# Kernel tuning notes

Hardware: AMD Instinct MI355X
Metric: run time of the kernel (lower is better)

Reference implementation:

```python
import jax, jax.numpy as jnp
import numpy as np

B, C_IN, C_OUT, L = 16, 512, 512, 2048
HEADS, K, U, KS, PAD = 4, 16, 1, 3, 1
VV = C_OUT // HEADS  # 128
EPS = 1e-5


def _conv1d(x, w, pad):
    # x: [B, Cin, L], w: [Cout, Cin, KS] -> [B, Cout, L]
    return jax.lax.conv_general_dilated(
        x, w, window_strides=(1,), padding=[(pad, pad)],
        dimension_numbers=('NCH', 'OIH', 'NCH'))


def _bn_eval(y, gamma, beta, mean, var):
    # inference-mode BatchNorm1d over channel axis
    scale = gamma * jax.lax.rsqrt(var + EPS)
    shift = beta - mean * scale
    return y * scale[None, :, None] + shift[None, :, None]


def setup_inputs() -> dict:
    key = jax.random.key(0)
    ks = jax.random.split(key, 8)
    std_q = 1.0 / np.sqrt(C_IN * KS)
    x = jax.random.normal(ks[0], (B, C_IN, L), dtype=jnp.float32)
    Wq = jax.random.normal(ks[1], (K * HEADS, C_IN, KS), dtype=jnp.float32) * std_q
    Wk = jax.random.normal(ks[2], (K * U, C_IN, KS), dtype=jnp.float32) * std_q
    Wv = jax.random.normal(ks[3], (VV * U, C_IN, KS), dtype=jnp.float32) * std_q
    embedding = jax.random.normal(ks[4], (K, U), dtype=jnp.float32)
    return {
        'x': x, 'Wq': Wq,
        'q_gamma': jnp.ones((K * HEADS,), jnp.float32),
        'q_beta': jnp.zeros((K * HEADS,), jnp.float32),
        'q_mean': jnp.zeros((K * HEADS,), jnp.float32),
        'q_var': jnp.ones((K * HEADS,), jnp.float32),
        'Wk': Wk, 'Wv': Wv,
        'v_gamma': jnp.ones((VV * U,), jnp.float32),
        'v_beta': jnp.zeros((VV * U,), jnp.float32),
        'v_mean': jnp.zeros((VV * U,), jnp.float32),
        'v_var': jnp.ones((VV * U,), jnp.float32),
        'embedding': embedding,
    }


def reference(x, Wq, q_gamma, q_beta, q_mean, q_var, Wk, Wv,
              v_gamma, v_beta, v_mean, v_var, embedding):
    batch, _, n = x.shape
    # projections
    q = _bn_eval(_conv1d(x, Wq, PAD), q_gamma, q_beta, q_mean, q_var)
    q = q.reshape(batch, HEADS, K, n)                      # bhkn
    keys = _conv1d(x, Wk, PAD).reshape(batch, K, U, n)     # bkun
    sm = jax.nn.softmax(keys, axis=-1)                     # softmax over positions
    v = _bn_eval(_conv1d(x, Wv, PAD), v_gamma, v_beta, v_mean, v_var)
    v = v.reshape(batch, VV, U, n)                         # bvun
    # content lambda
    lambda_c = jnp.einsum('bkun,bvun->bkv', sm, v)
    y_c = jnp.einsum('bhkn,bkv->bhvn', q, lambda_c)
    # position lambda
    lambda_p = jnp.einsum('ku,bvun->bkvn', embedding, v)
    y_p = jnp.einsum('bhkn,bkvn->bhvn', q, lambda_p)
    out = y_c + y_p
    return out.reshape(batch, HEADS * VV, n)
```

## Files before the change

kernel.cpp:

```cpp
#include <hip/hip_runtime.h>
#include <hip/hip_bf16.h>

#define BB 16
#define CIN 512
#define LL 2048
#define HEADS 4
#define KK 16
#define VVC 128
#define EPSV 1e-5f

typedef __attribute__((ext_vector_type(8))) short bf16x8s;
typedef __attribute__((ext_vector_type(4))) float f32x4;

__device__ __forceinline__ unsigned short f2bf(float f) {
    union { float f; unsigned int i; } c; c.f = f;
    unsigned int x = c.i;
    unsigned int lsb = (x >> 16) & 1;
    x += 0x7fff + lsb;
    return (unsigned short)(x >> 16);
}
__device__ __forceinline__ unsigned int pack2bf(float a, float b) {
    return (unsigned int)f2bf(a) | ((unsigned int)f2bf(b) << 16);
}

#define WCHUNK_U16 3840

__global__ __launch_bounds__(256) void prep_weights(
    const float* __restrict__ Wq, const float* __restrict__ Wk,
    const float* __restrict__ Wv, unsigned short* __restrict__ Wpk)
{
    int blk = blockIdx.x;
    int cot = blk >> 4, chunk = blk & 15;
    int ci0 = chunk * 32;
    for (int i = threadIdx.x; i < WCHUNK_U16; i += 256) {
        int t = i / 1280, r = i % 1280, co = r / 40, ci = r % 40;
        float val = 0.f;
        int cop = cot * 32 + co;
        if (ci < 32) {
            int cig = ci0 + ci;
            if (cop < 64)        val = Wq[((size_t)cop * 512 + cig) * 3 + t];
            else if (cop < 80)   val = Wk[((size_t)(cop - 64) * 512 + cig) * 3 + t];
            else if (cop < 208)  val = Wv[((size_t)(cop - 80) * 512 + cig) * 3 + t];
        }
        Wpk[(size_t)blk * WCHUNK_U16 + i] = f2bf(val);
    }
}

#define XSTRIDE 20

__global__ __launch_bounds__(256) void conv_mfma(
    const float* __restrict__ x, const unsigned short* __restrict__ Wpk,
    const float* __restrict__ qg, const float* __restrict__ qb,
    const float* __restrict__ qm, const float* __restrict__ qv,
    const float* __restrict__ vg, const float* __restrict__ vb,
    const float* __restrict__ vm, const float* __restrict__ vvar,
    float* __restrict__ qbuf, float* __restrict__ kbuf, float* __restrict__ vbuf)
{
    __shared__ __align__(16) unsigned int xT[258 * XSTRIDE];
    __shared__ __align__(16) unsigned short wA[WCHUNK_U16];
    __shared__ float sscale[32], sshift[32];

    const int tid = threadIdx.x;
    const int wave = tid >> 6, lane = tid & 63;
    const int kq = lane >> 4, lm = lane & 15;
    const int n0 = blockIdx.x * 256;
    const int cot = blockIdx.y;
    const int b = blockIdx.z;

    if (tid < 32) {
        int cop = cot * 32 + tid;
        float sc = 1.f, sh = 0.f;
        if (cop < 64) {
            float g = qg[cop], be = qb[cop], m = qm[cop], va = qv[cop];
            sc = g * rsqrtf(va + EPSV); sh = be - m * sc;
        } else if (cop >= 80 && cop < 208) {
            int c = cop - 80;
            float g = vg[c], be = vb[c], m = vm[c], va = vvar[c];
            sc = g * rsqrtf(va + EPSV); sh = be - m * sc;
        }
        sscale[tid] = sc; sshift[tid] = sh;
    }

    f32x4 acc[2][4];
#pragma unroll
    for (int i = 0; i < 2; i++)
#pragma unroll
        for (int j = 0; j < 4; j++) acc[i][j] = (f32x4){0.f, 0.f, 0.f, 0.f};

    const float* xb = x + (size_t)b * CIN * LL;

    for (int chunk = 0; chunk < 16; chunk++) {
        __syncthreads();
        {
            const uint4* src = (const uint4*)(Wpk + (size_t)(cot * 16 + chunk) * WCHUNK_U16);
            uint4* dst = (uint4*)wA;
            for (int i = tid; i < WCHUNK_U16 / 8; i += 256) dst[i] = src[i];
        }
        const int ci0 = chunk * 32;
        for (int i = tid; i < 4096; i += 256) {
            int p = i >> 8, nl = i & 255;
            float v0 = xb[(size_t)(ci0 + 2 * p) * LL + n0 + nl];
            float v1 = xb[(size_t)(ci0 + 2 * p + 1) * LL + n0 + nl];
            int row = nl + 1;
            int colp = p ^ (((row >> 2) & 3) << 2);
            xT[row * XSTRIDE + colp] = pack2bf(v0, v1);
        }
        if (tid < 32) {
            int p = tid >> 1, c = tid & 1;
            int gn = c ? (n0 + 256) : (n0 - 1);
            float v0 = 0.f, v1 = 0.f;
            if (gn >= 0 && gn < LL) {
                v0 = xb[(size_t)(ci0 + 2 * p) * LL + gn];
                v1 = xb[(size_t)(ci0 + 2 * p + 1) * LL + gn];
            }
            int row = c ? 257 : 0;
            int colp = p ^ (((row >> 2) & 3) << 2);
            xT[row * XSTRIDE + colp] = pack2bf(v0, v1);
        }
        __syncthreads();

#pragma unroll
        for (int t = 0; t < 3; t++) {
            bf16x8s aF0 = *(const bf16x8s*)&wA[t * 1280 + lm * 40 + kq * 8];
            bf16x8s aF1 = *(const bf16x8s*)&wA[t * 1280 + (16 + lm) * 40 + kq * 8];
#pragma unroll
            for (int fn = 0; fn < 4; fn++) {
                int row = wave * 64 + fn * 16 + lm + t;
                int cg = ((kq ^ ((row >> 2) & 3)) << 2);
                bf16x8s bF = *(const bf16x8s*)&xT[row * XSTRIDE + cg];
                acc[0][fn] = __builtin_amdgcn_mfma_f32_16x16x32_bf16(aF0, bF, acc[0][fn], 0, 0, 0);
                acc[1][fn] = __builtin_amdgcn_mfma_f32_16x16x32_bf16(aF1, bF, acc[1][fn], 0, 0, 0);
            }
        }
    }

#pragma unroll
    for (int cf = 0; cf < 2; cf++) {
#pragma unroll
        for (int fn = 0; fn < 4; fn++) {
#pragma unroll
            for (int r = 0; r < 4; r++) {
                int col = cf * 16 + kq * 4 + r;
                int cop = cot * 32 + col;
                if (cop >= 208) continue;
                float val = acc[cf][fn][r] * sscale[col] + sshift[col];
                int nout = n0 + wave * 64 + fn * 16 + lm;
                if (cop < 64)
                    qbuf[((size_t)b * 64 + cop) * LL + nout] = val;
                else if (cop < 80)
                    kbuf[((size_t)b * 16 + (cop - 64)) * LL + nout] = val;
                else
                    vbuf[((size_t)b * 128 + (cop - 80)) * LL + nout] = val;
            }
        }
    }
}

__global__ __launch_bounds__(256) void softmax_kernel(float* __restrict__ kbuf)
{
    const int row = blockIdx.x;
    float* p = kbuf + (size_t)row * LL;
    const int tid = threadIdx.x;
    __shared__ float red[256];

    float vals[8];
    float vmax = -1e30f;
#pragma unroll
    for (int j = 0; j < 8; j++) {
        vals[j] = p[tid + j * 256];
        vmax = fmaxf(vmax, vals[j]);
    }
    red[tid] = vmax;
    __syncthreads();
    for (int s = 128; s > 0; s >>= 1) {
        if (tid < s) red[tid] = fmaxf(red[tid], red[tid + s]);
        __syncthreads();
    }
    float m = red[0];
    __syncthreads();
    float sum = 0.f;
#pragma unroll
    for (int j = 0; j < 8; j++) {
        vals[j] = __expf(vals[j] - m);
        sum += vals[j];
    }
    red[tid] = sum;
    __syncthreads();
    for (int s = 128; s > 0; s >>= 1) {
        if (tid < s) red[tid] += red[tid + s];
        __syncthreads();
    }
    float inv = 1.f / red[0];
#pragma unroll
    for (int j = 0; j < 8; j++) p[tid + j * 256] = vals[j] * inv;
}

__global__ __launch_bounds__(256) void lambdac_kernel(
    const float* __restrict__ sm, const float* __restrict__ vbuf,
    float* __restrict__ lc)
{
    const int wave = threadIdx.x >> 6;
    const int lane = threadIdx.x & 63;
    const int task = blockIdx.x * 4 + wave;
    const int b = task >> 8;
    const int rem = task & 255;
    const int k = rem >> 4;
    const int vg = rem & 15;
    const float* ps = sm + ((size_t)b * 16 + k) * LL;
    const float* pv = vbuf + ((size_t)b * 128 + vg * 8) * LL;
    float acc[8];
#pragma unroll
    for (int i = 0; i < 8; i++) acc[i] = 0.f;
#pragma unroll
    for (int j = 0; j < 8; j++) {
        int n = (j * 64 + lane) * 4;
        float4 s4 = *(const float4*)&ps[n];
#pragma unroll
        for (int vi = 0; vi < 8; vi++) {
            float4 v4 = *(const float4*)&pv[(size_t)vi * LL + n];
            acc[vi] += s4.x * v4.x + s4.y * v4.y + s4.z * v4.z + s4.w * v4.w;
        }
    }
#pragma unroll
    for (int vi = 0; vi < 8; vi++) {
#pragma unroll
        for (int off = 32; off > 0; off >>= 1)
            acc[vi] += __shfl_xor(acc[vi], off, 64);
    }
    if (lane == 0) {
#pragma unroll
        for (int vi = 0; vi < 8; vi++)
            lc[((size_t)b * 16 + k) * 128 + vg * 8 + vi] = acc[vi];
    }
}

#define FT_N 256
__global__ __launch_bounds__(256) void final_kernel(
    const float* __restrict__ qbuf, const float* __restrict__ vbuf,
    const float* __restrict__ lc, const float* __restrict__ emb,
    float* __restrict__ out)
{
    __shared__ float qs[16][FT_N];
    __shared__ float lcs[16][128];
    __shared__ float es[16];
    const int tid = threadIdx.x;
    const int n0 = blockIdx.x * FT_N;
    const int h = blockIdx.y;
    const int b = blockIdx.z;

    for (int i = tid; i < 16 * FT_N; i += 256) {
        int r = i >> 8, c = i & 255;
        qs[r][c] = qbuf[((size_t)b * 64 + h * 16 + r) * LL + n0 + c];
    }
    for (int i = tid; i < 16 * 128; i += 256)
        lcs[i >> 7][i & 127] = lc[(size_t)b * 2048 + i];
    if (tid < 16) es[tid] = emb[tid];
    __syncthreads();

    const int n = n0 + tid;
    float q[16];
    float s = 0.f;
#pragma unroll
    for (int k2 = 0; k2 < 16; k2++) {
        q[k2] = qs[k2][tid];
        s += q[k2] * es[k2];
    }
    const float* pv = vbuf + (size_t)b * 128 * LL + n;
    float* po = out + ((size_t)b * 512 + h * 128) * LL + n;
    for (int v = 0; v < 128; v++) {
        float lam = 0.f;
#pragma unroll
        for (int k2 = 0; k2 < 16; k2++) lam += q[k2] * lcs[k2][v];
        float vvv = pv[(size_t)v * LL];
        po[(size_t)v * LL] = lam + s * vvv;
    }
}

extern "C" void kernel_launch(void* const* d_in, const int* in_sizes, int n_in,
                              void* d_out, int out_size, void* d_ws, size_t ws_size,
                              hipStream_t stream)
{
    const float* x   = (const float*)d_in[0];
    const float* Wq  = (const float*)d_in[1];
    const float* qg  = (const float*)d_in[2];
    const float* qb  = (const float*)d_in[3];
    const float* qm  = (const float*)d_in[4];
    const float* qv  = (const float*)d_in[5];
    const float* Wk  = (const float*)d_in[6];
    const float* Wv  = (const float*)d_in[7];
    const float* vg  = (const float*)d_in[8];
    const float* vb  = (const float*)d_in[9];
    const float* vm  = (const float*)d_in[10];
    const float* vva = (const float*)d_in[11];
    const float* emb = (const float*)d_in[12];
    float* out = (float*)d_out;

    float* qbuf = (float*)d_ws;
    float* kbuf = qbuf + (size_t)BB * 64 * LL;
    float* vbuf = kbuf + (size_t)BB * 16 * LL;
    float* lcb  = vbuf + (size_t)BB * 128 * LL;
    unsigned short* Wpk = (unsigned short*)(lcb + (size_t)BB * 16 * 128);

    hipLaunchKernelGGL(prep_weights, dim3(112), dim3(256), 0, stream, Wq, Wk, Wv, Wpk);

    hipLaunchKernelGGL(conv_mfma, dim3(8, 7, 16), dim3(256), 0, stream,
                       x, Wpk, qg, qb, qm, qv, vg, vb, vm, vva,
                       qbuf, kbuf, vbuf);

    hipLaunchKernelGGL(softmax_kernel, dim3(BB * 16), dim3(256), 0, stream, kbuf);

    hipLaunchKernelGGL(lambdac_kernel, dim3(1024), dim3(256), 0, stream,
                       kbuf, vbuf, lcb);

    hipLaunchKernelGGL(final_kernel, dim3(LL / FT_N, HEADS, BB), dim3(256), 0, stream,
                       qbuf, vbuf, lcb, emb, out);
}
```

Before: 233.7 us.

## Pre-pack x to bf16 and stream conv tiles via global_load_lds with wider tiles

Adds a prep_x kernel that converts x to bf16 once, in a pre-swizzled, halo-padded layout. The conv kernel can then copy its tiles straight into LDS with global_load_lds instead of converting fp32 per block. Each conv block now covers 64 output channels instead of 32, which gives more MFMA reuse per B fragment and fewer blocks re-reading x. The lambda_c kernel also processes 4 keys per wave so each V load is reused across them. The cost is an extra kernel launch and x round-tripping through memory, and the copy is still synchronous with no overlap.

```diff
diff --git a/kernel.cpp b/kernel.cpp
--- a/kernel.cpp
+++ b/kernel.cpp
@@ -1,12 +1,8 @@
 #include <hip/hip_runtime.h>
-#include <hip/hip_bf16.h>
 
 #define BB 16
 #define CIN 512
-#define LL 2048
-#define HEADS 4
-#define KK 16
-#define VVC 128
+#define LLN 2048
 #define EPSV 1e-5f
 
 typedef __attribute__((ext_vector_type(8))) short bf16x8s;
@@ -23,7 +19,13 @@
     return (unsigned int)f2bf(a) | ((unsigned int)f2bf(b) << 16);
 }
 
-#define WCHUNK_U16 3840
+__device__ __forceinline__ void g2l16(const void* g, void* l) {
+    typedef const __attribute__((address_space(1))) unsigned int GU;
+    typedef __attribute__((address_space(3))) unsigned int LU;
+    __builtin_amdgcn_global_load_lds((GU*)g, (LU*)l, 16, 0, 0);
+}
+
+#define WIMG_U16 7680
 
 __global__ __launch_bounds__(256) void prep_weights(
     const float* __restrict__ Wq, const float* __restrict__ Wk,
@@ -32,33 +34,59 @@
     int blk = blockIdx.x;
     int cot = blk >> 4, chunk = blk & 15;
     int ci0 = chunk * 32;
-    for (int i = threadIdx.x; i < WCHUNK_U16; i += 256) {
-        int t = i / 1280, r = i % 1280, co = r / 40, ci = r % 40;
+    for (int i = threadIdx.x; i < WIMG_U16; i += 256) {
+        int t = i / 2560, r = i % 2560, co = r / 40, ci = r % 40;
         float val = 0.f;
-        int cop = cot * 32 + co;
+        int cop = cot * 64 + co;
         if (ci < 32) {
             int cig = ci0 + ci;
             if (cop < 64)        val = Wq[((size_t)cop * 512 + cig) * 3 + t];
             else if (cop < 80)   val = Wk[((size_t)(cop - 64) * 512 + cig) * 3 + t];
             else if (cop < 208)  val = Wv[((size_t)(cop - 80) * 512 + cig) * 3 + t];
         }
-        Wpk[(size_t)blk * WCHUNK_U16 + i] = f2bf(val);
-    }
-}
-
-#define XSTRIDE 20
+        Wpk[(size_t)blk * WIMG_U16 + i] = f2bf(val);
+    }
+}
+
+__global__ __launch_bounds__(256) void prep_x(
+    const float* __restrict__ x, unsigned short* __restrict__ xpk)
+{
+    const int nt = blockIdx.x;
+    const int c  = blockIdx.y;
+    const int b  = blockIdx.z;
+    const int tid = threadIdx.x;
+    const int n = nt * 256 + tid;
+    const int rp = n + 1;
+    const float* xb = x + ((size_t)b * CIN + (size_t)c * 32) * LLN + n;
+    unsigned int row[16];
+#pragma unroll
+    for (int p = 0; p < 16; p++)
+        row[p] = pack2bf(xb[(size_t)(2 * p) * LLN], xb[(size_t)(2 * p + 1) * LLN]);
+    unsigned short* dst = xpk + ((size_t)(b * 16 + c) * 2050 + rp) * 32;
+    const int sig = (rp >> 1) & 3;
+#pragma unroll
+    for (int s = 0; s < 4; s++) {
+        int g = (s ^ sig) * 4;
+        uint4 v = make_uint4(row[g], row[g + 1], row[g + 2], row[g + 3]);
+        *(uint4*)(dst + s * 8) = v;
+    }
+    if (nt == 0 && tid < 4)
+        *(uint4*)(xpk + ((size_t)(b * 16 + c) * 2050) * 32 + tid * 8) = make_uint4(0, 0, 0, 0);
+    if (nt == 7 && tid < 4)
+        *(uint4*)(xpk + ((size_t)(b * 16 + c) * 2050 + 2049) * 32 + tid * 8) = make_uint4(0, 0, 0, 0);
+}
 
 __global__ __launch_bounds__(256) void conv_mfma(
-    const float* __restrict__ x, const unsigned short* __restrict__ Wpk,
+    const unsigned short* __restrict__ xpk, const unsigned short* __restrict__ Wpk,
     const float* __restrict__ qg, const float* __restrict__ qb,
     const float* __restrict__ qm, const float* __restrict__ qv,
     const float* __restrict__ vg, const float* __restrict__ vb,
     const float* __restrict__ vm, const float* __restrict__ vvar,
     float* __restrict__ qbuf, float* __restrict__ kbuf, float* __restrict__ vbuf)
 {
-    __shared__ __align__(16) unsigned int xT[258 * XSTRIDE];
-    __shared__ __align__(16) unsigned short wA[WCHUNK_U16];
-    __shared__ float sscale[32], sshift[32];
+    __shared__ __align__(16) unsigned short xT[258 * 32];
+    __shared__ __align__(16) unsigned short wA[WIMG_U16];
+    __shared__ float sscale[64], sshift[64];
 
     const int tid = threadIdx.x;
     const int wave = tid >> 6, lane = tid & 63;
@@ -67,90 +95,73 @@
     const int cot = blockIdx.y;
     const int b = blockIdx.z;
 
-    if (tid < 32) {
-        int cop = cot * 32 + tid;
+    if (tid < 64) {
+        int cop = cot * 64 + tid;
         float sc = 1.f, sh = 0.f;
         if (cop < 64) {
             float g = qg[cop], be = qb[cop], m = qm[cop], va = qv[cop];
             sc = g * rsqrtf(va + EPSV); sh = be - m * sc;
         } else if (cop >= 80 && cop < 208) {
-            int c = cop - 80;
-            float g = vg[c], be = vb[c], m = vm[c], va = vvar[c];
+            int cc = cop - 80;
+            float g = vg[cc], be = vb[cc], m = vm[cc], va = vvar[cc];
             sc = g * rsqrtf(va + EPSV); sh = be - m * sc;
         }
         sscale[tid] = sc; sshift[tid] = sh;
     }
 
-    f32x4 acc[2][4];
-#pragma unroll
-    for (int i = 0; i < 2; i++)
+    f32x4 acc[4][4];
+#pragma unroll
+    for (int i = 0; i < 4; i++)
 #pragma unroll
         for (int j = 0; j < 4; j++) acc[i][j] = (f32x4){0.f, 0.f, 0.f, 0.f};
-
-    const float* xb = x + (size_t)b * CIN * LL;
 
     for (int chunk = 0; chunk < 16; chunk++) {
         __syncthreads();
-        {
-            const uint4* src = (const uint4*)(Wpk + (size_t)(cot * 16 + chunk) * WCHUNK_U16);
-            uint4* dst = (uint4*)wA;
-            for (int i = tid; i < WCHUNK_U16 / 8; i += 256) dst[i] = src[i];
-        }
-        const int ci0 = chunk * 32;
-        for (int i = tid; i < 4096; i += 256) {
-            int p = i >> 8, nl = i & 255;
-            float v0 = xb[(size_t)(ci0 + 2 * p) * LL + n0 + nl];
-            float v1 = xb[(size_t)(ci0 + 2 * p + 1) * LL + n0 + nl];
-            int row = nl + 1;
-            int colp = p ^ (((row >> 2) & 3) << 2);
-            xT[row * XSTRIDE + colp] = pack2bf(v0, v1);
-        }
-        if (tid < 32) {
-            int p = tid >> 1, c = tid & 1;
-            int gn = c ? (n0 + 256) : (n0 - 1);
-            float v0 = 0.f, v1 = 0.f;
-            if (gn >= 0 && gn < LL) {
-                v0 = xb[(size_t)(ci0 + 2 * p) * LL + gn];
-                v1 = xb[(size_t)(ci0 + 2 * p + 1) * LL + gn];
+        const unsigned short* wsrc = Wpk + (size_t)(cot * 16 + chunk) * WIMG_U16;
+        const unsigned short* xsrc = xpk + ((size_t)(b * 16 + chunk) * 2050 + n0) * 32;
+        for (int i = tid; i < 960; i += 256)
+            g2l16(wsrc + (size_t)i * 8, wA + i * 8);
+        for (int i = tid; i < 1032; i += 256)
+            g2l16(xsrc + (size_t)i * 8, xT + i * 8);
+        asm volatile("s_waitcnt vmcnt(0)" ::: "memory");
+        __syncthreads();
+
+#pragma unroll
+        for (int t = 0; t < 3; t++) {
+            bf16x8s aF[4];
+#pragma unroll
+            for (int cf = 0; cf < 4; cf++)
+                aF[cf] = *(const bf16x8s*)&wA[t * 2560 + (cf * 16 + lm) * 40 + kq * 8];
+#pragma unroll
+            for (int fn = 0; fn < 4; fn++) {
+                int lr = wave * 64 + fn * 16 + lm + t;
+                int grp = kq ^ ((lr >> 1) & 3);
+                bf16x8s bF = *(const bf16x8s*)&xT[lr * 32 + grp * 8];
+#pragma unroll
+                for (int cf = 0; cf < 4; cf++)
+                    acc[cf][fn] = __builtin_amdgcn_mfma_f32_16x16x32_bf16(
+                        aF[cf], bF, acc[cf][fn], 0, 0, 0);
             }
-            int row = c ? 257 : 0;
-            int colp = p ^ (((row >> 2) & 3) << 2);
-            xT[row * XSTRIDE + colp] = pack2bf(v0, v1);
-        }
-        __syncthreads();
-
-#pragma unroll
-        for (int t = 0; t < 3; t++) {
-            bf16x8s aF0 = *(const bf16x8s*)&wA[t * 1280 + lm * 40 + kq * 8];
-            bf16x8s aF1 = *(const bf16x8s*)&wA[t * 1280 + (16 + lm) * 40 + kq * 8];
-#pragma unroll
-            for (int fn = 0; fn < 4; fn++) {
-                int row = wave * 64 + fn * 16 + lm + t;
-                int cg = ((kq ^ ((row >> 2) & 3)) << 2);
-                bf16x8s bF = *(const bf16x8s*)&xT[row * XSTRIDE + cg];
-                acc[0][fn] = __builtin_amdgcn_mfma_f32_16x16x32_bf16(aF0, bF, acc[0][fn], 0, 0, 0);
-                acc[1][fn] = __builtin_amdgcn_mfma_f32_16x16x32_bf16(aF1, bF, acc[1][fn], 0, 0, 0);
-            }
-        }
-    }
-
-#pragma unroll
-    for (int cf = 0; cf < 2; cf++) {
+        }
+    }
+
+#pragma unroll
+    for (int cf = 0; cf < 4; cf++) {
 #pragma unroll
         for (int fn = 0; fn < 4; fn++) {
 #pragma unroll
             for (int r = 0; r < 4; r++) {
                 int col = cf * 16 + kq * 4 + r;
-                int cop = cot * 32 + col;
+                int cop = cot * 64 + col;
                 if (cop >= 208) continue;
                 float val = acc[cf][fn][r] * sscale[col] + sshift[col];
                 int nout = n0 + wave * 64 + fn * 16 + lm;
                 if (cop < 64)
-                    qbuf[((size_t)b * 64 + cop) * LL + nout] = val;
+                    qbuf[((size_t)b * 64 + cop) * LLN + nout] = val;
                 else if (cop < 80)
-                    kbuf[((size_t)b * 16 + (cop - 64)) * LL + nout] = val;
+                    kbuf[((size_t)b * 16 + (cop - 64)) * LLN + nout] = val;
                 else
-                    vbuf[((size_t)b * 128 + (cop - 80)) * LL + nout] = val;
+                    vbuf[((size_t)b * 128 + (cop - 80)) * LLN + nout] = val;
             }
         }
     }
@@ -159,7 +170,7 @@
 __global__ __launch_bounds__(256) void softmax_kernel(float* __restrict__ kbuf)
 {
     const int row = blockIdx.x;
-    float* p = kbuf + (size_t)row * LL;
+    float* p = kbuf + (size_t)row * LLN;
     const int tid = threadIdx.x;
     __shared__ float red[256];
 
@@ -201,36 +212,44 @@
 {
     const int wave = threadIdx.x >> 6;
     const int lane = threadIdx.x & 63;
-    const int task = blockIdx.x * 4 + wave;
-    const int b = task >> 8;
-    const int rem = task & 255;
-    const int k = rem >> 4;
-    const int vg = rem & 15;
-    const float* ps = sm + ((size_t)b * 16 + k) * LL;
-    const float* pv = vbuf + ((size_t)b * 128 + vg * 8) * LL;
-    float acc[8];
-#pragma unroll
-    for (int i = 0; i < 8; i++) acc[i] = 0.f;
+    const int b = blockIdx.x >> 4;
+    const int vg = blockIdx.x & 15;
+    const float* ps = sm + ((size_t)b * 16 + wave * 4) * LLN;
+    const float* pv = vbuf + ((size_t)b * 128 + vg * 8) * LLN;
+    float acc[4][8];
+#pragma unroll
+    for (int k = 0; k < 4; k++)
+#pragma unroll
+        for (int v = 0; v < 8; v++) acc[k][v] = 0.f;
 #pragma unroll
     for (int j = 0; j < 8; j++) {
         int n = (j * 64 + lane) * 4;
-        float4 s4 = *(const float4*)&ps[n];
-#pragma unroll
-        for (int vi = 0; vi < 8; vi++) {
-            float4 v4 = *(const float4*)&pv[(size_t)vi * LL + n];
-            acc[vi] += s4.x * v4.x + s4.y * v4.y + s4.z * v4.z + s4.w * v4.w;
-        }
-    }
-#pragma unroll
-    for (int vi = 0; vi < 8; vi++) {
-#pragma unroll
-        for (int off = 32; off > 0; off >>= 1)
-            acc[vi] += __shfl_xor(acc[vi], off, 64);
-    }
+        float4 s4[4], v4[8];
+#pragma unroll
+        for (int k = 0; k < 4; k++) s4[k] = *(const float4*)&ps[(size_t)k * LLN + n];
+#pragma unroll
+        for (int v = 0; v < 8; v++) v4[v] = *(const float4*)&pv[(size_t)v * LLN + n];
+#pragma unroll
+        for (int k = 0; k < 4; k++)
+#pragma unroll
+            for (int v = 0; v < 8; v++)
+                acc[k][v] += s4[k].x * v4[v].x + s4[k].y * v4[v].y
+                           + s4[k].z * v4[v].z + s4[k].w * v4[v].w;
+    }
+#pragma unroll
+    for (int k = 0; k < 4; k++)
+#pragma unroll
+        for (int v = 0; v < 8; v++) {
+#pragma unroll
+            for (int off = 32; off > 0; off >>= 1)
+                acc[k][v] += __shfl_xor(acc[k][v], off, 64);
+        }
     if (lane == 0) {
 #pragma unroll
-        for (int vi = 0; vi < 8; vi++)
-            lc[((size_t)b * 16 + k) * 128 + vg * 8 + vi] = acc[vi];
+        for (int k = 0; k < 4; k++)
+#pragma unroll
+            for (int v = 0; v < 8; v++)
+                lc[((size_t)b * 16 + wave * 4 + k) * 128 + vg * 8 + v] = acc[k][v];
     }
 }
 
@@ -250,7 +269,7 @@
 
     for (int i = tid; i < 16 * FT_N; i += 256) {
         int r = i >> 8, c = i & 255;
-        qs[r][c] = qbuf[((size_t)b * 64 + h * 16 + r) * LL + n0 + c];
+        qs[r][c] = qbuf[((size_t)b * 64 + h * 16 + r) * LLN + n0 + c];
     }
     for (int i = tid; i < 16 * 128; i += 256)
         lcs[i >> 7][i & 127] = lc[(size_t)b * 2048 + i];
@@ -265,14 +284,14 @@
         q[k2] = qs[k2][tid];
         s += q[k2] * es[k2];
     }
-    const float* pv = vbuf + (size_t)b * 128 * LL + n;
-    float* po = out + ((size_t)b * 512 + h * 128) * LL + n;
+    const float* pv = vbuf + (size_t)b * 128 * LLN + n;
+    float* po = out + ((size_t)b * 512 + h * 128) * LLN + n;
     for (int v = 0; v < 128; v++) {
         float lam = 0.f;
 #pragma unroll
         for (int k2 = 0; k2 < 16; k2++) lam += q[k2] * lcs[k2][v];
-        float vvv = pv[(size_t)v * LL];
-        po[(size_t)v * LL] = lam + s * vvv;
+        float vvv = pv[(size_t)v * LLN];
+        po[(size_t)v * LLN] = lam + s * vvv;
     }
 }
 
@@ -296,22 +315,25 @@
     float* out = (float*)d_out;
 
     float* qbuf = (float*)d_ws;
-    float* kbuf = qbuf + (size_t)BB * 64 * LL;
-    float* vbuf = kbuf + (size_t)BB * 16 * LL;
-    float* lcb  = vbuf + (size_t)BB * 128 * LL;
+    float* kbuf = qbuf + (size_t)BB * 64 * LLN;
+    float* vbuf = kbuf + (size_t)BB * 16 * LLN;
+    float* lcb  = vbuf + (size_t)BB * 128 * LLN;
     unsigned short* Wpk = (unsigned short*)(lcb + (size_t)BB * 16 * 128);
-
-    hipLaunchKernelGGL(prep_weights, dim3(112), dim3(256), 0, stream, Wq, Wk, Wv, Wpk);
-
-    hipLaunchKernelGGL(conv_mfma, dim3(8, 7, 16), dim3(256), 0, stream,
-                       x, Wpk, qg, qb, qm, qv, vg, vb, vm, vva,
+    unsigned short* xpk = Wpk + (size_t)64 * WIMG_U16;
+
+    hipLaunchKernelGGL(prep_weights, dim3(64), dim3(256), 0, stream, Wq, Wk, Wv, Wpk);
+
+    hipLaunchKernelGGL(prep_x, dim3(8, 16, 16), dim3(256), 0, stream, x, xpk);
+
+    hipLaunchKernelGGL(conv_mfma, dim3(8, 4, 16), dim3(256), 0, stream,
+                       xpk, Wpk, qg, qb, qm, qv, vg, vb, vm, vva,
                        qbuf, kbuf, vbuf);
 
     hipLaunchKernelGGL(softmax_kernel, dim3(BB * 16), dim3(256), 0, stream, kbuf);
 
-    hipLaunchKernelGGL(lambdac_kernel, dim3(1024), dim3(256), 0, stream,
+    hipLaunchKernelGGL(lambdac_kernel, dim3(256), dim3(256), 0, stream,
                        kbuf, vbuf, lcb);
 
-    hipLaunchKernelGGL(final_kernel, dim3(LL / FT_N, HEADS, BB), dim3(256), 0, stream,
+    hipLaunchKernelGGL(final_kernel, dim3(LLN / FT_N, 4, BB), dim3(256), 0, stream,
                        qbuf, vbuf, lcb, emb, out);
 }
```

New measurement: 213.8 us. -8.5%, faster.
